# Performance work log

Hardware: AMD Instinct MI355X
Metric: run time of the kernel (lower is better)

The kernel has to match this reference:

```python
import jax, jax.numpy as jnp
import numpy as np

B, S, D, H = 2, 2048, 512, 8
HD = D // H
SPARSITY = 0.15
KTOP = max(1, int(S * SPARSITY))          # 307 important rows
HALF_WIN = min(32, S // 4) // 2           # 16 -> window |i-j| <= 16
RC = min(16, S // 8)                      # 16 random links per query token


def setup_inputs() -> dict:
    key = jax.random.key(0)
    ks = jax.random.split(key, 8)
    s = 0.02
    return {
        "x":  jax.random.normal(ks[0], (B, S, D), jnp.float32),
        "Wq": jax.random.normal(ks[1], (D, D), jnp.float32) * s,
        "bq": jnp.zeros((D,), jnp.float32),
        "Wk": jax.random.normal(ks[2], (D, D), jnp.float32) * s,
        "bk": jnp.zeros((D,), jnp.float32),
        "Wv": jax.random.normal(ks[3], (D, D), jnp.float32) * s,
        "bv": jnp.zeros((D,), jnp.float32),
        "Wo": jax.random.normal(ks[4], (D, D), jnp.float32) * s,
        "bo": jnp.zeros((D,), jnp.float32),
        "Ws1": jax.random.normal(ks[5], (D, D // 2), jnp.float32) * s,
        "bs1": jnp.zeros((D // 2,), jnp.float32),
        "Ws2": jax.random.normal(ks[6], (D // 2, 1), jnp.float32) * s,
        "bs2": jnp.zeros((1,), jnp.float32),
        # models torch.randperm(S)[:RC] per (b, i); duplicates are harmless for set-to-1
        "rand_idx": jax.random.randint(ks[7], (B, S, RC), 0, S, jnp.int32),
    }


def _sparse_mask(x, Ws1, bs1, Ws2, bs2, rand_idx):
    # importance scorer: Linear -> ReLU -> Linear -> Sigmoid, squeeze(-1)
    imp = jax.nn.sigmoid(jax.nn.relu(x @ Ws1 + bs1) @ Ws2 + bs2)[..., 0]  # [B,S]
    _, top_idx = jax.lax.top_k(imp, KTOP)                                  # [B,KTOP]
    brange = jnp.arange(B)
    row_imp = jnp.zeros((B, S), bool).at[brange[:, None], top_idx].set(True)
    idx = jnp.arange(S)
    win = jnp.abs(idx[:, None] - idx[None, :]) <= HALF_WIN                 # [S,S]
    rmask = jnp.zeros((B, S, S), bool).at[
        brange[:, None, None], idx[None, :, None], rand_idx].set(True)    # [B,S,S]
    mask = row_imp[:, :, None] | win[None, :, :] | rmask                   # [B,S,S]
    tril = idx[:, None] >= idx[None, :]                                    # causal (mask * (causal==0))
    return mask & tril


def reference(x, Wq, bq, Wk, bk, Wv, bv, Wo, bo, Ws1, bs1, Ws2, bs2, rand_idx):
    allowed = _sparse_mask(x, Ws1, bs1, Ws2, bs2, rand_idx)                # [B,S,S] bool
    q = (x @ Wq + bq).reshape(B, S, H, HD).transpose(0, 2, 1, 3)           # [B,H,S,HD]
    k = (x @ Wk + bk).reshape(B, S, H, HD).transpose(0, 2, 1, 3)
    v = (x @ Wv + bv).reshape(B, S, H, HD).transpose(0, 2, 1, 3)
    scores = jnp.einsum('bhid,bhjd->bhij', q, k) / jnp.sqrt(jnp.float32(HD))
    scores = jnp.where(allowed[:, None, :, :], scores, -jnp.inf)
    attn = jax.nn.softmax(scores, axis=-1)                                 # every row has j=i allowed
    out = jnp.einsum('bhij,bhjd->bhid', attn, v)
    out = out.transpose(0, 2, 1, 3).reshape(B, S, D)
    return out @ Wo + bo
```

## Files before the change

### kernel.cpp

```cpp
#include <hip/hip_runtime.h>
#include <math.h>

typedef unsigned short u16;
typedef unsigned int u32;
typedef unsigned long long u64;
typedef short bf16x8 __attribute__((ext_vector_type(8)));
typedef float f32x4 __attribute__((ext_vector_type(4)));

constexpr int NB = 2, NS = 2048, ND = 512, NH = 8, NHD = 64;
constexpr int NKTOP = 307, NHWIN = 16, NRC = 16;
constexpr int NILIST = 320;
constexpr int NSPAR = NS - NKTOP;
constexpr int NSPAD = 1744;
constexpr int NCHUNK = 8;
constexpr int LDSPAD = 40;
constexpr int LDSK64 = 72;
constexpr int PSTR = 72;

__device__ __forceinline__ u16 f2bf(float f) {
  u32 u = __builtin_bit_cast(u32, f);
  u32 r = (u + 0x7FFFu + ((u >> 16) & 1u)) >> 16;
  return (u16)r;
}
__device__ __forceinline__ float bf2f(short v) {
  return __builtin_bit_cast(float, (u32)(u16)v << 16);
}

__global__ __launch_bounds__(256) void csa_cvt_w(const float* __restrict__ W0, const float* __restrict__ W1,
                                                 const float* __restrict__ W2, const float* __restrict__ W3,
                                                 u16* __restrict__ wt) {
  __shared__ float tile[64][33];
  int w = blockIdx.z;
  const float* src = (w == 0) ? W0 : (w == 1) ? W1 : (w == 2) ? W2 : W3;
  int kb = blockIdx.x * 64, nb = blockIdx.y * 32;
  int tx = threadIdx.x & 31, ty = threadIdx.x >> 5;
  for (int i = ty; i < 64; i += 8) tile[i][tx] = src[(size_t)(kb + i) * ND + nb + tx];
  __syncthreads();
  u16* dst = wt + (size_t)w * ND * ND;
  for (int n = ty; n < 32; n += 8) {
    u32 pk = (u32)f2bf(tile[2 * tx][n]) | ((u32)f2bf(tile[2 * tx + 1][n]) << 16);
    *(u32*)(&dst[(size_t)(nb + n) * ND + kb + 2 * tx]) = pk;
  }
}

__global__ __launch_bounds__(256) void csa_scorer(const float* __restrict__ x, const float* __restrict__ Ws1,
                                                  const float* __restrict__ bs1, const float* __restrict__ Ws2,
                                                  float* __restrict__ part) {
  __shared__ float As[32][68];
  __shared__ float Bs[32][68];
  const int tid = threadIdx.x;
  const int m0 = blockIdx.x * 64, n0 = blockIdx.y * 64;
  const int ty = tid >> 4, tx = tid & 15;
  float acc[4][4] = {};
  const int arow = tid & 63, aks = (tid >> 6) * 8;
  const int bk = tid >> 3, bc = (tid & 7) * 8;
  for (int k0 = 0; k0 < ND; k0 += 32) {
    __syncthreads();
    {
      float4 a0 = *(const float4*)(&x[(size_t)(m0 + arow) * ND + k0 + aks]);
      float4 a1 = *(const float4*)(&x[(size_t)(m0 + arow) * ND + k0 + aks + 4]);
      As[aks + 0][arow] = a0.x; As[aks + 1][arow] = a0.y;
      As[aks + 2][arow] = a0.z; As[aks + 3][arow] = a0.w;
      As[aks + 4][arow] = a1.x; As[aks + 5][arow] = a1.y;
      As[aks + 6][arow] = a1.z; As[aks + 7][arow] = a1.w;
    }
    *(float4*)(&Bs[bk][bc]) = *(const float4*)(&Ws1[(size_t)(k0 + bk) * 256 + n0 + bc]);
    *(float4*)(&Bs[bk][bc + 4]) = *(const float4*)(&Ws1[(size_t)(k0 + bk) * 256 + n0 + bc + 4]);
    __syncthreads();
    for (int k = 0; k < 32; k++) {
      float4 av = *(const float4*)(&As[k][ty * 4]);
      float4 bv = *(const float4*)(&Bs[k][tx * 4]);
      float aa[4] = {av.x, av.y, av.z, av.w};
      float bb[4] = {bv.x, bv.y, bv.z, bv.w};
      for (int i = 0; i < 4; i++)
        for (int j = 0; j < 4; j++)
          acc[i][j] += aa[i] * bb[j];
    }
  }
  float4 w2 = *(const float4*)(&Ws2[n0 + tx * 4]);
  float4 b1 = *(const float4*)(&bs1[n0 + tx * 4]);
  for (int i = 0; i < 4; i++) {
    float p = fmaxf(acc[i][0] + b1.x, 0.f) * w2.x + fmaxf(acc[i][1] + b1.y, 0.f) * w2.y +
              fmaxf(acc[i][2] + b1.z, 0.f) * w2.z + fmaxf(acc[i][3] + b1.w, 0.f) * w2.w;
    for (int off = 1; off < 16; off <<= 1) p += __shfl_xor(p, off, 64);
    if (tx == 0) part[(size_t)(m0 + ty * 4 + i) * 4 + blockIdx.y] = p;
  }
}

__global__ __launch_bounds__(256) void csa_rank(const float* __restrict__ part, int* __restrict__ rowimp) {
  __shared__ float vals[NS];
  const int b = blockIdx.y;
  {
    int t8 = threadIdx.x * 8;
    for (int e = 0; e < 8; e++) {
      float4 pp = *(const float4*)(&part[(size_t)(b * NS + t8 + e) * 4]);
      vals[t8 + e] = (pp.x + pp.y) + (pp.z + pp.w);
    }
  }
  __syncthreads();
  const int wave = threadIdx.x >> 6, lane = threadIdx.x & 63;
  const int s0 = blockIdx.x * 8 + wave * 2;
  const int s1 = s0 + 1;
  const float v0 = vals[s0], v1 = vals[s1];
  int r0 = 0, r1 = 0;
  for (int t = lane; t < NS; t += 64) {
    float u = vals[t];
    r0 += (int)((u > v0) | ((u == v0) & (t < s0)));
    r1 += (int)((u > v1) | ((u == v1) & (t < s1)));
  }
  for (int off = 1; off < 64; off <<= 1) {
    r0 += __shfl_xor(r0, off, 64);
    r1 += __shfl_xor(r1, off, 64);
  }
  if (lane == 0) {
    rowimp[b * NS + s0] = (r0 < NKTOP) ? 1 : 0;
    rowimp[b * NS + s1] = (r1 < NKTOP) ? 1 : 0;
  }
}

__global__ __launch_bounds__(256) void csa_ilist(const int* __restrict__ rowimp, int* __restrict__ ilist,
                                                 int* __restrict__ nlist) {
  __shared__ int cs[256];
  int b = blockIdx.x, t = threadIdx.x;
  int flags[8], sum = 0;
  for (int k = 0; k < 8; k++) {
    flags[k] = rowimp[b * NS + t * 8 + k];
    sum += flags[k];
  }
  cs[t] = sum;
  __syncthreads();
  for (int off = 1; off < 256; off <<= 1) {
    int v = (t >= off) ? cs[t - off] : 0;
    __syncthreads();
    cs[t] += v;
    __syncthreads();
  }
  int pos = cs[t] - sum;
  for (int k = 0; k < 8; k++) {
    int r = t * 8 + k;
    if (flags[k]) ilist[b * NILIST + pos++] = r;
    else nlist[b * NSPAD + (r - pos)] = r;
  }
  if (t < NILIST - NKTOP) ilist[b * NILIST + NKTOP + t] = -1;
  if (t < NSPAD - NSPAR) nlist[b * NSPAD + NSPAR + t] = -1;
}

__global__ __launch_bounds__(256) void csa_gemm_qkv(const float* __restrict__ x, const u16* __restrict__ Bt,
                                                    const float* __restrict__ bq, const float* __restrict__ bk,
                                                    const float* __restrict__ bv, u16* __restrict__ qb,
                                                    u16* __restrict__ kb, u16* __restrict__ vtb,
                                                    u16* __restrict__ vb) {
  __shared__ __attribute__((aligned(16))) u16 As[128 * LDSPAD];
  __shared__ __attribute__((aligned(16))) u16 Bs[64 * LDSPAD];
  const int tid = threadIdx.x;
  const int wave = tid >> 6, lane = tid & 63;
  const int quad = lane >> 4, col = lane & 15;
  const int m0 = blockIdx.x * 128;
  const int n0 = blockIdx.y * 64;
  const f32x4 zf = {0.f, 0.f, 0.f, 0.f};
  f32x4 acc[2][4] = {{zf, zf, zf, zf}, {zf, zf, zf, zf}};
  const int sar = tid >> 1, sak = (tid & 1) * 16;
  const int sbr = tid >> 2, sbk = (tid & 3) * 8;
  for (int k0 = 0; k0 < ND; k0 += 32) {
    __syncthreads();
    {
      const float* xp = &x[(size_t)(m0 + sar) * ND + k0 + sak];
      float4 v0 = *(const float4*)(xp), v1 = *(const float4*)(xp + 4);
      float4 v2 = *(const float4*)(xp + 8), v3 = *(const float4*)(xp + 12);
      u32 w0 = (u32)f2bf(v0.x) | ((u32)f2bf(v0.y) << 16);
      u32 w1 = (u32)f2bf(v0.z) | ((u32)f2bf(v0.w) << 16);
      u32 w2 = (u32)f2bf(v1.x) | ((u32)f2bf(v1.y) << 16);
      u32 w3 = (u32)f2bf(v1.z) | ((u32)f2bf(v1.w) << 16);
      u32 w4 = (u32)f2bf(v2.x) | ((u32)f2bf(v2.y) << 16);
      u32 w5 = (u32)f2bf(v2.z) | ((u32)f2bf(v2.w) << 16);
      u32 w6 = (u32)f2bf(v3.x) | ((u32)f2bf(v3.y) << 16);
      u32 w7 = (u32)f2bf(v3.z) | ((u32)f2bf(v3.w) << 16);
      u32* ap = (u32*)&As[sar * LDSPAD + sak];
      ap[0] = w0; ap[1] = w1; ap[2] = w2; ap[3] = w3;
      ap[4] = w4; ap[5] = w5; ap[6] = w6; ap[7] = w7;
    }
    *(uint4*)(&Bs[sbr * LDSPAD + sbk]) = *(const uint4*)(&Bt[(size_t)(n0 + sbr) * ND + k0 + sbk]);
    __syncthreads();
    bf16x8 af0 = *(const bf16x8*)(&As[(wave * 32 + col) * LDSPAD + quad * 8]);
    bf16x8 af1 = *(const bf16x8*)(&As[(wave * 32 + 16 + col) * LDSPAD + quad * 8]);
    for (int c = 0; c < 4; c++) {
      bf16x8 bfr = *(const bf16x8*)(&Bs[(c * 16 + col) * LDSPAD + quad * 8]);
      acc[0][c] = __builtin_amdgcn_mfma_f32_16x16x32_bf16(af0, bfr, acc[0][c], 0, 0, 0);
      acc[1][c] = __builtin_amdgcn_mfma_f32_16x16x32_bf16(af1, bfr, acc[1][c], 0, 0, 0);
    }
  }
  const int w = n0 >> 9;
  const float* bias = (w == 0) ? bq : (w == 1) ? bk : bv;
  for (int c = 0; c < 4; c++) {
    const int ng = n0 + c * 16 + col;
    const int nn = ng & 511, hh = nn >> 6, hd = nn & 63;
    const float bvv = bias[nn];
    for (int r = 0; r < 2; r++) {
      for (int rr = 0; rr < 4; rr++) {
        const int m = m0 + wave * 32 + r * 16 + quad * 4 + rr;
        const int bb = m >> 11, s = m & (NS - 1);
        u16 v16 = f2bf(acc[r][c][rr] + bvv);
        if (w == 0) qb[((size_t)(bb * NH + hh) * NS + s) * NHD + hd] = v16;
        else if (w == 1) kb[((size_t)(bb * NH + hh) * NS + s) * NHD + hd] = v16;
        else {
          vtb[((size_t)(bb * NH + hh) * NHD + hd) * NS + s] = v16;
          vb[((size_t)(bb * NH + hh) * NS + s) * NHD + hd] = v16;
        }
      }
    }
  }
}

__global__ __launch_bounds__(256) void csa_gemm_out(const u16* __restrict__ A, const u16* __restrict__ Bt,
                                                    const float* __restrict__ bias, float* __restrict__ outp) {
  __shared__ __attribute__((aligned(16))) u16 As[64 * LDSK64];
  __shared__ __attribute__((aligned(16))) u16 Bs[64 * LDSK64];
  const int tid = threadIdx.x;
  const int wave = tid >> 6, lane = tid & 63;
  const int quad = lane >> 4, col = lane & 15;
  const int m0 = blockIdx.x * 64;
  const int n0 = blockIdx.y * 64;
  const f32x4 zf = {0.f, 0.f, 0.f, 0.f};
  f32x4 acc[4] = {zf, zf, zf, zf};
  const int sr = tid >> 2, sk = (tid & 3) * 16;
  for (int k0 = 0; k0 < ND; k0 += 64) {
    __syncthreads();
    *(uint4*)(&As[sr * LDSK64 + sk]) = *(const uint4*)(&A[(size_t)(m0 + sr) * ND + k0 + sk]);
    *(uint4*)(&As[sr * LDSK64 + sk + 8]) = *(const uint4*)(&A[(size_t)(m0 + sr) * ND + k0 + sk + 8]);
    *(uint4*)(&Bs[sr * LDSK64 + sk]) = *(const uint4*)(&Bt[(size_t)(n0 + sr) * ND + k0 + sk]);
    *(uint4*)(&Bs[sr * LDSK64 + sk + 8]) = *(const uint4*)(&Bt[(size_t)(n0 + sr) * ND + k0 + sk + 8]);
    __syncthreads();
    bf16x8 af0 = *(const bf16x8*)(&As[(wave * 16 + col) * LDSK64 + quad * 8]);
    bf16x8 af1 = *(const bf16x8*)(&As[(wave * 16 + col) * LDSK64 + 32 + quad * 8]);
    for (int nt = 0; nt < 4; nt++) {
      bf16x8 bf0 = *(const bf16x8*)(&Bs[(nt * 16 + col) * LDSK64 + quad * 8]);
      bf16x8 bf1 = *(const bf16x8*)(&Bs[(nt * 16 + col) * LDSK64 + 32 + quad * 8]);
      acc[nt] = __builtin_amdgcn_mfma_f32_16x16x32_bf16(af0, bf0, acc[nt], 0, 0, 0);
      acc[nt] = __builtin_amdgcn_mfma_f32_16x16x32_bf16(af1, bf1, acc[nt], 0, 0, 0);
    }
  }
  for (int nt = 0; nt < 4; nt++) {
    const int n = n0 + nt * 16 + col;
    const float bvv = bias[n];
    for (int r = 0; r < 4; r++) {
      const int m = m0 + wave * 16 + quad * 4 + r;
      outp[(size_t)m * ND + n] = acc[nt][r] + bvv;
    }
  }
}

__global__ __launch_bounds__(64) void csa_attn_imp(const u16* __restrict__ qb, const u16* __restrict__ kb,
                                                   const u16* __restrict__ vtb, const int* __restrict__ ilist,
                                                   float* __restrict__ pbuf) {
  const int lane = threadIdx.x;
  const int quad = lane >> 4, col = lane & 15;
  const int qt = blockIdx.x;
  const int chunk = blockIdx.y;
  const int bh = blockIdx.z;
  const int b = bh >> 3, h = bh & 7;

  const int* il = ilist + b * NILIST;
  const u16* qptr = qb + (size_t)(b * NH + h) * NS * NHD;
  const u16* kptr = kb + (size_t)(b * NH + h) * NS * NHD;
  const u16* vptr = vtb + (size_t)(b * NH + h) * NHD * NS;

  const int iq = il[qt * 16 + col];
  const int qrow = (iq < 0) ? 0 : iq;
  bf16x8 qf0 = *(const bf16x8*)(qptr + qrow * NHD + quad * 8);
  bf16x8 qf1 = *(const bf16x8*)(qptr + qrow * NHD + 32 + quad * 8);

  const f32x4 zf = {0.f, 0.f, 0.f, 0.f};
  float m_r[4], l_r[4];
  f32x4 of[4];
  int irow[4];
  for (int r = 0; r < 4; r++) {
    m_r[r] = -INFINITY;
    l_r[r] = 0.f;
    irow[r] = il[qt * 16 + quad * 4 + r];
  }
  for (int n = 0; n < 4; n++) of[n] = zf;

  __shared__ __attribute__((aligned(16))) u16 Pl[16 * PSTR];

  const int max_i = il[(qt * 16 + 15 > NKTOP - 1) ? (NKTOP - 1) : (qt * 16 + 15)];
  const int ntiles = (max_i >> 6) + 1;
  for (int t = chunk; t < ntiles; t += NCHUNK) {
    const int j0 = t * 64;
    f32x4 cg[4];
    for (int g = 0; g < 4; g++) {
      const int jb = j0 + g * 16;
      bf16x8 k0f = *(const bf16x8*)(kptr + (jb + col) * NHD + quad * 8);
      bf16x8 k1f = *(const bf16x8*)(kptr + (jb + col) * NHD + 32 + quad * 8);
      f32x4 c = zf;
      c = __builtin_amdgcn_mfma_f32_16x16x32_bf16(qf0, k0f, c, 0, 0, 0);
      c = __builtin_amdgcn_mfma_f32_16x16x32_bf16(qf1, k1f, c, 0, 0, 0);
      cg[g] = c;
    }
    float ps[4][4], alpha[4];
    for (int r = 0; r < 4; r++) {
      const int i = irow[r];
      float s[4];
      float vmax = -INFINITY;
      for (int g = 0; g < 4; g++) {
        s[g] = (j0 + g * 16 + col <= i) ? cg[g][r] * 0.125f : -INFINITY;
        vmax = fmaxf(vmax, s[g]);
      }
      for (int off = 1; off < 16; off <<= 1) vmax = fmaxf(vmax, __shfl_xor(vmax, off, 64));
      float newm = fmaxf(m_r[r], vmax);
      bool dead = (newm == -INFINITY);
      float a = dead ? 1.f : __expf(m_r[r] - newm);
      float psum = 0.f;
      for (int g = 0; g < 4; g++) {
        float p = dead ? 0.f : __expf(s[g] - newm);
        ps[r][g] = p;
        psum += p;
      }
      for (int off = 1; off < 16; off <<= 1) psum += __shfl_xor(psum, off, 64);
      m_r[r] = newm;
      l_r[r] = l_r[r] * a + psum;
      alpha[r] = a;
    }
    for (int n = 0; n < 4; n++)
      for (int r = 0; r < 4; r++) of[n][r] *= alpha[r];
    __syncthreads();
    for (int r = 0; r < 4; r++)
      for (int g = 0; g < 4; g++)
        Pl[(quad * 4 + r) * PSTR + g * 16 + col] = f2bf(ps[r][g]);
    __syncthreads();
    bf16x8 pf0 = *(const bf16x8*)(&Pl[col * PSTR + quad * 8]);
    bf16x8 pf1 = *(const bf16x8*)(&Pl[col * PSTR + 32 + quad * 8]);
    for (int vn = 0; vn < 4; vn++) {
      bf16x8 vf0 = *(const bf16x8*)(vptr + (size_t)(vn * 16 + col) * NS + j0 + quad * 8);
      bf16x8 vf1 = *(const bf16x8*)(vptr + (size_t)(vn * 16 + col) * NS + j0 + 32 + quad * 8);
      of[vn] = __builtin_amdgcn_mfma_f32_16x16x32_bf16(pf0, vf0, of[vn], 0, 0, 0);
      of[vn] = __builtin_amdgcn_mfma_f32_16x16x32_bf16(pf1, vf1, of[vn], 0, 0, 0);
    }
  }
  float* pr = pbuf + ((size_t)(bh * NCHUNK + chunk) * NILIST + qt * 16) * 66;
  for (int r = 0; r < 4; r++) {
    const int row = quad * 4 + r;
    if (col == 0) {
      pr[row * 66 + 0] = m_r[r];
      pr[row * 66 + 1] = l_r[r];
    }
    for (int vn = 0; vn < 4; vn++)
      pr[row * 66 + 2 + vn * 16 + col] = of[vn][r];
  }
}

__global__ __launch_bounds__(64) void csa_merge(const float* __restrict__ pbuf, const int* __restrict__ ilist,
                                                u16* __restrict__ attnb) {
  const int kp = blockIdx.x, h = blockIdx.y, b = blockIdx.z;
  const int lane = threadIdx.x;
  const int z = b * NH + h;
  float mc[NCHUNK], lc[NCHUNK], mstar = -INFINITY;
  for (int c = 0; c < NCHUNK; c++) {
    const float* base = pbuf + ((size_t)(z * NCHUNK + c) * NILIST + kp) * 66;
    mc[c] = base[0];
    lc[c] = base[1];
    mstar = fmaxf(mstar, mc[c]);
  }
  float lsum = 0.f, osum = 0.f;
  for (int c = 0; c < NCHUNK; c++) {
    const float* base = pbuf + ((size_t)(z * NCHUNK + c) * NILIST + kp) * 66;
    float w = (mc[c] == -INFINITY) ? 0.f : __expf(mc[c] - mstar);
    lsum += w * lc[c];
    osum += w * base[2 + lane];
  }
  const int i = ilist[b * NILIST + kp];
  attnb[((size_t)(b * NS + i) * NH + h) * NHD + lane] = f2bf(osum / lsum);
}

__global__ __launch_bounds__(256) void csa_attn_sparse(const u16* __restrict__ qb, const u16* __restrict__ kb,
                                                       const u16* __restrict__ vb, const int* __restrict__ nlist,
                                                       const int* __restrict__ rand_idx, u16* __restrict__ attnb) {
  __shared__ __attribute__((aligned(16))) u16 ql[4][64];
  __shared__ float pl[4][33];
  __shared__ int jl[4][33];
  const int wave = threadIdx.x >> 6, lane = threadIdx.x & 63;
  const int slot = blockIdx.x * 4 + wave;
  const int h = blockIdx.y, b = blockIdx.z;
  const int i = nlist[b * NSPAD + slot];
  const int iv = (i < 0) ? 0 : i;

  const u16* qrow = qb + ((size_t)(b * NH + h) * NS + iv) * NHD;
  const u16* kbase = kb + (size_t)(b * NH + h) * NS * NHD;
  const u16* vbase = vb + (size_t)(b * NH + h) * NS * NHD;

  if (lane < 8) *(bf16x8*)(&ql[wave][lane * 8]) = *(const bf16x8*)(qrow + lane * 8);
  __syncthreads();

  float sd = bf2f((short)ql[wave][lane]) * bf2f((short)kbase[(size_t)iv * NHD + lane]);
  for (int off = 1; off < 64; off <<= 1) sd += __shfl_xor(sd, off, 64);
  sd *= 0.125f;

  const int c = lane >> 1, half = lane & 1;
  int j, valid;
  if (c < 16) {
    j = i - NHWIN + c;
    valid = (j >= 0);
  } else {
    const int* rr = rand_idx + ((size_t)b * NS + iv) * NRC;
    const int cr = c - 16;
    j = rr[cr];
    valid = (j <= i - NHWIN - 1);
    for (int cp = 0; cp < cr; cp++) valid &= (rr[cp] != j);
  }
  const int jr = valid ? j : 0;
  float s = 0.f;
  {
    const u16* krow = kbase + (size_t)jr * NHD + half * 32;
    for (int c8 = 0; c8 < 4; c8++) {
      bf16x8 kv = *(const bf16x8*)(krow + c8 * 8);
      bf16x8 qv = *(const bf16x8*)(&ql[wave][half * 32 + c8 * 8]);
      for (int e = 0; e < 8; e++) s += bf2f(qv[e]) * bf2f(kv[e]);
    }
  }
  s += __shfl_xor(s, 1, 64);
  s = valid ? s * 0.125f : -INFINITY;

  float smax = s;
  for (int off = 1; off < 64; off <<= 1) smax = fmaxf(smax, __shfl_xor(smax, off, 64));
  smax = fmaxf(smax, sd);
  float p = valid ? __expf(s - smax) : 0.f;
  float pd = __expf(sd - smax);
  float pm = (half == 0) ? p : 0.f;
  for (int off = 1; off < 64; off <<= 1) pm += __shfl_xor(pm, off, 64);
  const float lsum = pm + pd;

  if (half == 0) {
    pl[wave][c] = p;
    jl[wave][c] = jr;
  }
  if (lane == 0) {
    pl[wave][32] = pd;
    jl[wave][32] = iv;
  }
  __syncthreads();

  float o = 0.f;
  for (int jj = 0; jj < 33; jj++) {
    const int jk = __builtin_amdgcn_readfirstlane(jl[wave][jj]);
    const float pj = pl[wave][jj];
    o += pj * bf2f((short)vbase[(size_t)jk * NHD + lane]);
  }
  if (i >= 0)
    attnb[((size_t)(b * NS + i) * NH + h) * NHD + lane] = f2bf(o / lsum);
}

extern "C" void kernel_launch(void* const* d_in, const int* in_sizes, int n_in,
                              void* d_out, int out_size, void* d_ws, size_t ws_size,
                              hipStream_t stream) {
  const float* x = (const float*)d_in[0];
  const float* bq = (const float*)d_in[2];
  const float* bk = (const float*)d_in[4];
  const float* bv = (const float*)d_in[6];
  const float* bo = (const float*)d_in[8];
  const float* Ws1 = (const float*)d_in[9];
  const float* bs1 = (const float*)d_in[10];
  const float* Ws2 = (const float*)d_in[11];
  const int* rand_idx = (const int*)d_in[13];
  float* out = (float*)d_out;

  char* p = (char*)d_ws;
  u16* wt = (u16*)p;         p += (size_t)4 * ND * ND * 2;
  u16* qbuf = (u16*)p;       p += (size_t)NB * NH * NS * NHD * 2;
  u16* kbuf = (u16*)p;       p += (size_t)NB * NH * NS * NHD * 2;
  u16* vtbuf = (u16*)p;      p += (size_t)NB * NH * NHD * NS * 2;
  u16* vbuf = (u16*)p;       p += (size_t)NB * NH * NS * NHD * 2;
  u16* attnb = (u16*)p;      p += (size_t)NB * NS * ND * 2;
  float* part = (float*)p;   p += (size_t)NB * NS * 4 * 4;
  int* rowimp = (int*)p;     p += (size_t)NB * NS * 4;
  int* ilist = (int*)p;      p += (size_t)NB * NILIST * 4;
  int* nlist = (int*)p;      p += (size_t)NB * NSPAD * 4;
  float* pbuf = (float*)p;

  csa_cvt_w<<<dim3(8, 16, 4), 256, 0, stream>>>((const float*)d_in[1], (const float*)d_in[3],
                                                (const float*)d_in[5], (const float*)d_in[7], wt);

  csa_scorer<<<dim3(NB * NS / 64, 4), 256, 0, stream>>>(x, Ws1, bs1, Ws2, part);
  csa_rank<<<dim3(NS / 8, NB), 256, 0, stream>>>(part, rowimp);
  csa_ilist<<<dim3(NB), 256, 0, stream>>>(rowimp, ilist, nlist);

  csa_gemm_qkv<<<dim3(32, 24), 256, 0, stream>>>(x, wt, bq, bk, bv, qbuf, kbuf, vtbuf, vbuf);

  csa_attn_imp<<<dim3(NILIST / 16, NCHUNK, NB * NH), 64, 0, stream>>>(qbuf, kbuf, vtbuf, ilist, pbuf);
  csa_attn_sparse<<<dim3(NSPAD / 4, NH, NB), 256, 0, stream>>>(qbuf, kbuf, vbuf, nlist, rand_idx, attnb);
  csa_merge<<<dim3(NKTOP, NH, NB), 64, 0, stream>>>(pbuf, ilist, attnb);

  csa_gemm_out<<<dim3(64, 8), 256, 0, stream>>>(attnb, wt + 3 * (size_t)ND * ND, bo, out);
}
```

Baseline: 209.5 us.

## Fuse prep kernels, pre-convert x to bf16, deepen QKV K-tile, drop LDS in sparse attn

Merges weight conversion and the importance scorer into one launch, and adds a block range that converts x to bf16 once. The QKV GEMM then reads bf16 x directly and uses a 64-wide K step with two MFMAs per fragment, which halves the loop iterations and barriers. The sparse attention kernel drops its shared-memory staging and barrier, reading q from global memory and broadcasting probabilities and indices through wave shuffles. This trades an extra bf16 copy of x in the workspace and a larger LDS footprint for fewer launches and less conversion and synchronisation work.

```diff
diff --git a/kernel.cpp b/kernel.cpp
--- a/kernel.cpp
+++ b/kernel.cpp
@@ -13,7 +13,6 @@
 constexpr int NSPAR = NS - NKTOP;
 constexpr int NSPAD = 1744;
 constexpr int NCHUNK = 8;
-constexpr int LDSPAD = 40;
 constexpr int LDSK64 = 72;
 constexpr int PSTR = 72;
 
@@ -26,64 +25,78 @@
   return __builtin_bit_cast(float, (u32)(u16)v << 16);
 }
 
-__global__ __launch_bounds__(256) void csa_cvt_w(const float* __restrict__ W0, const float* __restrict__ W1,
-                                                 const float* __restrict__ W2, const float* __restrict__ W3,
-                                                 u16* __restrict__ wt) {
-  __shared__ float tile[64][33];
-  int w = blockIdx.z;
-  const float* src = (w == 0) ? W0 : (w == 1) ? W1 : (w == 2) ? W2 : W3;
-  int kb = blockIdx.x * 64, nb = blockIdx.y * 32;
-  int tx = threadIdx.x & 31, ty = threadIdx.x >> 5;
-  for (int i = ty; i < 64; i += 8) tile[i][tx] = src[(size_t)(kb + i) * ND + nb + tx];
-  __syncthreads();
-  u16* dst = wt + (size_t)w * ND * ND;
-  for (int n = ty; n < 32; n += 8) {
-    u32 pk = (u32)f2bf(tile[2 * tx][n]) | ((u32)f2bf(tile[2 * tx + 1][n]) << 16);
-    *(u32*)(&dst[(size_t)(nb + n) * ND + kb + 2 * tx]) = pk;
-  }
-}
-
-__global__ __launch_bounds__(256) void csa_scorer(const float* __restrict__ x, const float* __restrict__ Ws1,
-                                                  const float* __restrict__ bs1, const float* __restrict__ Ws2,
-                                                  float* __restrict__ part) {
-  __shared__ float As[32][68];
-  __shared__ float Bs[32][68];
+__global__ __launch_bounds__(256) void csa_prep(const float* __restrict__ W0, const float* __restrict__ W1,
+                                                const float* __restrict__ W2, const float* __restrict__ W3,
+                                                u16* __restrict__ wt, const float* __restrict__ x,
+                                                u16* __restrict__ xb, const float* __restrict__ Ws1,
+                                                const float* __restrict__ bs1, const float* __restrict__ Ws2,
+                                                float* __restrict__ part) {
+  __shared__ float sh[2 * 32 * 68];
   const int tid = threadIdx.x;
-  const int m0 = blockIdx.x * 64, n0 = blockIdx.y * 64;
-  const int ty = tid >> 4, tx = tid & 15;
-  float acc[4][4] = {};
-  const int arow = tid & 63, aks = (tid >> 6) * 8;
-  const int bk = tid >> 3, bc = (tid & 7) * 8;
-  for (int k0 = 0; k0 < ND; k0 += 32) {
-    __syncthreads();
-    {
-      float4 a0 = *(const float4*)(&x[(size_t)(m0 + arow) * ND + k0 + aks]);
-      float4 a1 = *(const float4*)(&x[(size_t)(m0 + arow) * ND + k0 + aks + 4]);
-      As[aks + 0][arow] = a0.x; As[aks + 1][arow] = a0.y;
-      As[aks + 2][arow] = a0.z; As[aks + 3][arow] = a0.w;
-      As[aks + 4][arow] = a1.x; As[aks + 5][arow] = a1.y;
-      As[aks + 6][arow] = a1.z; As[aks + 7][arow] = a1.w;
-    }
-    *(float4*)(&Bs[bk][bc]) = *(const float4*)(&Ws1[(size_t)(k0 + bk) * 256 + n0 + bc]);
-    *(float4*)(&Bs[bk][bc + 4]) = *(const float4*)(&Ws1[(size_t)(k0 + bk) * 256 + n0 + bc + 4]);
-    __syncthreads();
-    for (int k = 0; k < 32; k++) {
-      float4 av = *(const float4*)(&As[k][ty * 4]);
-      float4 bv = *(const float4*)(&Bs[k][tx * 4]);
-      float aa[4] = {av.x, av.y, av.z, av.w};
-      float bb[4] = {bv.x, bv.y, bv.z, bv.w};
-      for (int i = 0; i < 4; i++)
-        for (int j = 0; j < 4; j++)
-          acc[i][j] += aa[i] * bb[j];
-    }
-  }
-  float4 w2 = *(const float4*)(&Ws2[n0 + tx * 4]);
-  float4 b1 = *(const float4*)(&bs1[n0 + tx * 4]);
-  for (int i = 0; i < 4; i++) {
-    float p = fmaxf(acc[i][0] + b1.x, 0.f) * w2.x + fmaxf(acc[i][1] + b1.y, 0.f) * w2.y +
-              fmaxf(acc[i][2] + b1.z, 0.f) * w2.z + fmaxf(acc[i][3] + b1.w, 0.f) * w2.w;
-    for (int off = 1; off < 16; off <<= 1) p += __shfl_xor(p, off, 64);
-    if (tx == 0) part[(size_t)(m0 + ty * 4 + i) * 4 + blockIdx.y] = p;
+  if (blockIdx.x < 256) {
+    const int m0 = (blockIdx.x & 63) * 64, n0 = (blockIdx.x >> 6) * 64;
+    float(*As)[68] = (float(*)[68])sh;
+    float(*Bs)[68] = (float(*)[68])(sh + 32 * 68);
+    const int ty = tid >> 4, tx = tid & 15;
+    float acc[4][4] = {};
+    const int arow = tid & 63, aks = (tid >> 6) * 8;
+    const int bk = tid >> 3, bc = (tid & 7) * 8;
+    for (int k0 = 0; k0 < ND; k0 += 32) {
+      __syncthreads();
+      {
+        float4 a0 = *(const float4*)(&x[(size_t)(m0 + arow) * ND + k0 + aks]);
+        float4 a1 = *(const float4*)(&x[(size_t)(m0 + arow) * ND + k0 + aks + 4]);
+        As[aks + 0][arow] = a0.x; As[aks + 1][arow] = a0.y;
+        As[aks + 2][arow] = a0.z; As[aks + 3][arow] = a0.w;
+        As[aks + 4][arow] = a1.x; As[aks + 5][arow] = a1.y;
+        As[aks + 6][arow] = a1.z; As[aks + 7][arow] = a1.w;
+      }
+      *(float4*)(&Bs[bk][bc]) = *(const float4*)(&Ws1[(size_t)(k0 + bk) * 256 + n0 + bc]);
+      *(float4*)(&Bs[bk][bc + 4]) = *(const float4*)(&Ws1[(size_t)(k0 + bk) * 256 + n0 + bc + 4]);
+      __syncthreads();
+      for (int k = 0; k < 32; k++) {
+        float4 av = *(const float4*)(&As[k][ty * 4]);
+        float4 bv = *(const float4*)(&Bs[k][tx * 4]);
+        float aa[4] = {av.x, av.y, av.z, av.w};
+        float bb[4] = {bv.x, bv.y, bv.z, bv.w};
+        for (int i = 0; i < 4; i++)
+          for (int j = 0; j < 4; j++)
+            acc[i][j] += aa[i] * bb[j];
+      }
+    }
+    float4 w2 = *(const float4*)(&Ws2[n0 + tx * 4]);
+    float4 b1 = *(const float4*)(&bs1[n0 + tx * 4]);
+    for (int i = 0; i < 4; i++) {
+      float p = fmaxf(acc[i][0] + b1.x, 0.f) * w2.x + fmaxf(acc[i][1] + b1.y, 0.f) * w2.y +
+                fmaxf(acc[i][2] + b1.z, 0.f) * w2.z + fmaxf(acc[i][3] + b1.w, 0.f) * w2.w;
+      for (int off = 1; off < 16; off <<= 1) p += __shfl_xor(p, off, 64);
+      if (tx == 0) part[(size_t)(m0 + ty * 4 + i) * 4 + (blockIdx.x >> 6)] = p;
+    }
+  } else if (blockIdx.x < 768) {
+    const int cb = blockIdx.x - 256;
+    const int w = cb >> 7;
+    const int kb = ((cb & 127) >> 4) * 64;
+    const int nb = (cb & 15) * 32;
+    const float* src = (w == 0) ? W0 : (w == 1) ? W1 : (w == 2) ? W2 : W3;
+    float(*tile)[33] = (float(*)[33])sh;
+    int tx = tid & 31, ty = tid >> 5;
+    for (int i = ty; i < 64; i += 8) tile[i][tx] = src[(size_t)(kb + i) * ND + nb + tx];
+    __syncthreads();
+    u16* dst = wt + (size_t)w * ND * ND;
+    for (int n = ty; n < 32; n += 8) {
+      u32 pk = (u32)f2bf(tile[2 * tx][n]) | ((u32)f2bf(tile[2 * tx + 1][n]) << 16);
+      *(u32*)(&dst[(size_t)(nb + n) * ND + kb + 2 * tx]) = pk;
+    }
+  } else {
+    const int i = ((blockIdx.x - 768) * 256 + tid) * 8;
+    float4 v0 = *(const float4*)(x + i);
+    float4 v1 = *(const float4*)(x + i + 4);
+    u32 o0 = (u32)f2bf(v0.x) | ((u32)f2bf(v0.y) << 16);
+    u32 o1 = (u32)f2bf(v0.z) | ((u32)f2bf(v0.w) << 16);
+    u32 o2 = (u32)f2bf(v1.x) | ((u32)f2bf(v1.y) << 16);
+    u32 o3 = (u32)f2bf(v1.z) | ((u32)f2bf(v1.w) << 16);
+    uint4 o = {o0, o1, o2, o3};
+    *(uint4*)(xb + i) = o;
   }
 }
 
@@ -145,13 +158,13 @@
   if (t < NSPAD - NSPAR) nlist[b * NSPAD + NSPAR + t] = -1;
 }
 
-__global__ __launch_bounds__(256) void csa_gemm_qkv(const float* __restrict__ x, const u16* __restrict__ Bt,
+__global__ __launch_bounds__(256) void csa_gemm_qkv(const u16* __restrict__ xb, const u16* __restrict__ Bt,
                                                     const float* __restrict__ bq, const float* __restrict__ bk,
                                                     const float* __restrict__ bv, u16* __restrict__ qb,
                                                     u16* __restrict__ kb, u16* __restrict__ vtb,
                                                     u16* __restrict__ vb) {
-  __shared__ __attribute__((aligned(16))) u16 As[128 * LDSPAD];
-  __shared__ __attribute__((aligned(16))) u16 Bs[64 * LDSPAD];
+  __shared__ __attribute__((aligned(16))) u16 As[128 * LDSK64];
+  __shared__ __attribute__((aligned(16))) u16 Bs[64 * LDSK64];
   const int tid = threadIdx.x;
   const int wave = tid >> 6, lane = tid & 63;
   const int quad = lane >> 4, col = lane & 15;
@@ -159,34 +172,32 @@
   const int n0 = blockIdx.y * 64;
   const f32x4 zf = {0.f, 0.f, 0.f, 0.f};
   f32x4 acc[2][4] = {{zf, zf, zf, zf}, {zf, zf, zf, zf}};
-  const int sar = tid >> 1, sak = (tid & 1) * 16;
-  const int sbr = tid >> 2, sbk = (tid & 3) * 8;
-  for (int k0 = 0; k0 < ND; k0 += 32) {
+  const int sar = tid >> 1, sak = (tid & 1) * 32;
+  const int sbr = tid >> 2, sbk = (tid & 3) * 16;
+  for (int k0 = 0; k0 < ND; k0 += 64) {
     __syncthreads();
     {
-      const float* xp = &x[(size_t)(m0 + sar) * ND + k0 + sak];
-      float4 v0 = *(const float4*)(xp), v1 = *(const float4*)(xp + 4);
-      float4 v2 = *(const float4*)(xp + 8), v3 = *(const float4*)(xp + 12);
-      u32 w0 = (u32)f2bf(v0.x) | ((u32)f2bf(v0.y) << 16);
-      u32 w1 = (u32)f2bf(v0.z) | ((u32)f2bf(v0.w) << 16);
-      u32 w2 = (u32)f2bf(v1.x) | ((u32)f2bf(v1.y) << 16);
-      u32 w3 = (u32)f2bf(v1.z) | ((u32)f2bf(v1.w) << 16);
-      u32 w4 = (u32)f2bf(v2.x) | ((u32)f2bf(v2.y) << 16);
-      u32 w5 = (u32)f2bf(v2.z) | ((u32)f2bf(v2.w) << 16);
-      u32 w6 = (u32)f2bf(v3.x) | ((u32)f2bf(v3.y) << 16);
-      u32 w7 = (u32)f2bf(v3.z) | ((u32)f2bf(v3.w) << 16);
-      u32* ap = (u32*)&As[sar * LDSPAD + sak];
-      ap[0] = w0; ap[1] = w1; ap[2] = w2; ap[3] = w3;
-      ap[4] = w4; ap[5] = w5; ap[6] = w6; ap[7] = w7;
-    }
-    *(uint4*)(&Bs[sbr * LDSPAD + sbk]) = *(const uint4*)(&Bt[(size_t)(n0 + sbr) * ND + k0 + sbk]);
-    __syncthreads();
-    bf16x8 af0 = *(const bf16x8*)(&As[(wave * 32 + col) * LDSPAD + quad * 8]);
-    bf16x8 af1 = *(const bf16x8*)(&As[(wave * 32 + 16 + col) * LDSPAD + quad * 8]);
+      const u16* xp = &xb[(size_t)(m0 + sar) * ND + k0 + sak];
+      u16* ap = &As[sar * LDSK64 + sak];
+      *(uint4*)(ap) = *(const uint4*)(xp);
+      *(uint4*)(ap + 8) = *(const uint4*)(xp + 8);
+      *(uint4*)(ap + 16) = *(const uint4*)(xp + 16);
+      *(uint4*)(ap + 24) = *(const uint4*)(xp + 24);
+    }
+    *(uint4*)(&Bs[sbr * LDSK64 + sbk]) = *(const uint4*)(&Bt[(size_t)(n0 + sbr) * ND + k0 + sbk]);
+    *(uint4*)(&Bs[sbr * LDSK64 + sbk + 8]) = *(const uint4*)(&Bt[(size_t)(n0 + sbr) * ND + k0 + sbk + 8]);
+    __syncthreads();
+    bf16x8 af[2][2];
+    for (int r = 0; r < 2; r++)
+      for (int hh = 0; hh < 2; hh++)
+        af[r][hh] = *(const bf16x8*)(&As[(wave * 32 + r * 16 + col) * LDSK64 + hh * 32 + quad * 8]);
     for (int c = 0; c < 4; c++) {
-      bf16x8 bfr = *(const bf16x8*)(&Bs[(c * 16 + col) * LDSPAD + quad * 8]);
-      acc[0][c] = __builtin_amdgcn_mfma_f32_16x16x32_bf16(af0, bfr, acc[0][c], 0, 0, 0);
-      acc[1][c] = __builtin_amdgcn_mfma_f32_16x16x32_bf16(af1, bfr, acc[1][c], 0, 0, 0);
+      bf16x8 b0 = *(const bf16x8*)(&Bs[(c * 16 + col) * LDSK64 + quad * 8]);
+      bf16x8 b1 = *(const bf16x8*)(&Bs[(c * 16 + col) * LDSK64 + 32 + quad * 8]);
+      acc[0][c] = __builtin_amdgcn_mfma_f32_16x16x32_bf16(af[0][0], b0, acc[0][c], 0, 0, 0);
+      acc[0][c] = __builtin_amdgcn_mfma_f32_16x16x32_bf16(af[0][1], b1, acc[0][c], 0, 0, 0);
+      acc[1][c] = __builtin_amdgcn_mfma_f32_16x16x32_bf16(af[1][0], b0, acc[1][c], 0, 0, 0);
+      acc[1][c] = __builtin_amdgcn_mfma_f32_16x16x32_bf16(af[1][1], b1, acc[1][c], 0, 0, 0);
     }
   }
   const int w = n0 >> 9;
@@ -374,9 +385,6 @@
 __global__ __launch_bounds__(256) void csa_attn_sparse(const u16* __restrict__ qb, const u16* __restrict__ kb,
                                                        const u16* __restrict__ vb, const int* __restrict__ nlist,
                                                        const int* __restrict__ rand_idx, u16* __restrict__ attnb) {
-  __shared__ __attribute__((aligned(16))) u16 ql[4][64];
-  __shared__ float pl[4][33];
-  __shared__ int jl[4][33];
   const int wave = threadIdx.x >> 6, lane = threadIdx.x & 63;
   const int slot = blockIdx.x * 4 + wave;
   const int h = blockIdx.y, b = blockIdx.z;
@@ -387,10 +395,7 @@
   const u16* kbase = kb + (size_t)(b * NH + h) * NS * NHD;
   const u16* vbase = vb + (size_t)(b * NH + h) * NS * NHD;
 
-  if (lane < 8) *(bf16x8*)(&ql[wave][lane * 8]) = *(const bf16x8*)(qrow + lane * 8);
-  __syncthreads();
-
-  float sd = bf2f((short)ql[wave][lane]) * bf2f((short)kbase[(size_t)iv * NHD + lane]);
+  float sd = bf2f((short)qrow[lane]) * bf2f((short)kbase[(size_t)iv * NHD + lane]);
   for (int off = 1; off < 64; off <<= 1) sd += __shfl_xor(sd, off, 64);
   sd *= 0.125f;
 
@@ -410,9 +415,10 @@
   float s = 0.f;
   {
     const u16* krow = kbase + (size_t)jr * NHD + half * 32;
+    const u16* qh = qrow + half * 32;
     for (int c8 = 0; c8 < 4; c8++) {
       bf16x8 kv = *(const bf16x8*)(krow + c8 * 8);
-      bf16x8 qv = *(const bf16x8*)(&ql[wave][half * 32 + c8 * 8]);
+      bf16x8 qv = *(const bf16x8*)(qh + c8 * 8);
       for (int e = 0; e < 8; e++) s += bf2f(qv[e]) * bf2f(kv[e]);
     }
   }
@@ -428,20 +434,11 @@
   for (int off = 1; off < 64; off <<= 1) pm += __shfl_xor(pm, off, 64);
   const float lsum = pm + pd;
 
-  if (half == 0) {
-    pl[wave][c] = p;
-    jl[wave][c] = jr;
-  }
-  if (lane == 0) {
-    pl[wave][32] = pd;
-    jl[wave][32] = iv;
-  }
-  __syncthreads();
-
-  float o = 0.f;
-  for (int jj = 0; jj < 33; jj++) {
-    const int jk = __builtin_amdgcn_readfirstlane(jl[wave][jj]);
-    const float pj = pl[wave][jj];
+  float o = pd * bf2f((short)vbase[(size_t)iv * NHD + lane]);
+#pragma unroll
+  for (int jj = 0; jj < 32; jj++) {
+    const float pj = __shfl(p, 2 * jj, 64);
+    const int jk = __shfl(jr, 2 * jj, 64);
     o += pj * bf2f((short)vbase[(size_t)jk * NHD + lane]);
   }
   if (i >= 0)
@@ -464,6 +461,7 @@
 
   char* p = (char*)d_ws;
   u16* wt = (u16*)p;         p += (size_t)4 * ND * ND * 2;
+  u16* xb = (u16*)p;         p += (size_t)NB * NS * ND * 2;
   u16* qbuf = (u16*)p;       p += (size_t)NB * NH * NS * NHD * 2;
   u16* kbuf = (u16*)p;       p += (size_t)NB * NH * NS * NHD * 2;
   u16* vtbuf = (u16*)p;      p += (size_t)NB * NH * NHD * NS * 2;
@@ -475,14 +473,13 @@
   int* nlist = (int*)p;      p += (size_t)NB * NSPAD * 4;
   float* pbuf = (float*)p;
 
-  csa_cvt_w<<<dim3(8, 16, 4), 256, 0, stream>>>((const float*)d_in[1], (const float*)d_in[3],
-                                                (const float*)d_in[5], (const float*)d_in[7], wt);
-
-  csa_scorer<<<dim3(NB * NS / 64, 4), 256, 0, stream>>>(x, Ws1, bs1, Ws2, part);
+  csa_prep<<<dim3(1792), 256, 0, stream>>>((const float*)d_in[1], (const float*)d_in[3],
+                                           (const float*)d_in[5], (const float*)d_in[7], wt,
+                                           x, xb, Ws1, bs1, Ws2, part);
   csa_rank<<<dim3(NS / 8, NB), 256, 0, stream>>>(part, rowimp);
   csa_ilist<<<dim3(NB), 256, 0, stream>>>(rowimp, ilist, nlist);
 
-  csa_gemm_qkv<<<dim3(32, 24), 256, 0, stream>>>(x, wt, bq, bk, bv, qbuf, kbuf, vtbuf, vbuf);
+  csa_gemm_qkv<<<dim3(32, 24), 256, 0, stream>>>(xb, wt, bq, bk, bv, qbuf, kbuf, vtbuf, vbuf);
 
   csa_attn_imp<<<dim3(NILIST / 16, NCHUNK, NB * NH), 64, 0, stream>>>(qbuf, kbuf, vtbuf, ilist, pbuf);
   csa_attn_sparse<<<dim3(NSPAD / 4, NH, NB), 256, 0, stream>>>(qbuf, kbuf, vbuf, nlist, rand_idx, attnb);
```

New measurement: 216.0 us. +3.1%, slower.
